# Optimization experiments

Measured on AMD Instinct MI355X. Metric: run time of the kernel, lower is better.

## Reference

```python
import jax, jax.numpy as jnp
import numpy as np

B, S, NN = 16, 512, 8          # batch, spatial nodes, neighbors per node
IN, H, NHEAD = 128, 512, 4     # input_size, hidden_size, n_head


def _forward(inputs, h, c, h_spatial, a_src, w_fg, b_fg, w_ig, b_ig,
             w_ih, w_hh, b_ih, b_hh):
    N = B * S
    x = inputs.reshape(N, IN)
    h = h.reshape(N, H)
    c = c.reshape(N, H)
    hs = h_spatial.reshape(N, NN, H)

    # attention logits: concat(h, neighbor) @ a_src, split to avoid materializing concat
    a_self, a_nb = a_src[:H], a_src[H:]              # [H, NHEAD] each
    attn = h @ a_self                                  # [N, NHEAD]
    attn = attn[:, None, :] + jnp.einsum('nkh,hm->nkm', hs, a_nb)  # [N, NN, NHEAD]
    attn = jnp.where(attn >= 0, attn, 0.2 * attn)      # leaky_relu(0.2)
    attn = jax.nn.softmax(attn, axis=1)                # softmax over neighbors

    # aggregate neighbors per head -> [N, NHEAD*H]
    agg = jnp.einsum('nkm,nkh->nmh', attn, hs).reshape(N, NHEAD * H)

    spatial_f = jax.nn.sigmoid(agg @ w_fg.T + b_fg)    # [N, H]
    spatial_i = jax.nn.sigmoid(agg @ w_ig.T + b_ig)
    h = h * spatial_i
    c = c * spatial_f

    # torch LSTMCell: gate order i, f, g, o
    gates = x @ w_ih.T + b_ih + h @ w_hh.T + b_hh      # [N, 4H]
    i_g, f_g, g_g, o_g = jnp.split(gates, 4, axis=1)
    i_g = jax.nn.sigmoid(i_g)
    f_g = jax.nn.sigmoid(f_g)
    g_g = jnp.tanh(g_g)
    o_g = jax.nn.sigmoid(o_g)
    c_new = f_g * c + i_g * g_g
    h_new = o_g * jnp.tanh(c_new)
    return h_new.reshape(B, S, H), c_new.reshape(B, S, H)


def setup_inputs() -> dict:
    key = jax.random.key(0)
    ks = jax.random.split(key, 16)
    xav = lambda k, shp: jax.random.uniform(
        k, shp, jnp.float32, -1.0, 1.0) * np.sqrt(6.0 / (shp[0] + shp[1]))
    return {
        'inputs': jax.random.normal(ks[0], (B, S, IN), jnp.float32),
        'h': jax.random.normal(ks[1], (B, S, H), jnp.float32),
        'c': jax.random.normal(ks[2], (B, S, H), jnp.float32),
        'h_spatial': jax.random.normal(ks[3], (B, S, NN, H), jnp.float32),
        'a_src': xav(ks[4], (2 * H, NHEAD)),
        'w_fg': jax.random.normal(ks[5], (H, NHEAD * H), jnp.float32) * 0.02,
        'b_fg': jnp.zeros((H,), jnp.float32),
        'w_ig': jax.random.normal(ks[6], (H, NHEAD * H), jnp.float32) * 0.02,
        'b_ig': jnp.zeros((H,), jnp.float32),
        'w_ih': jax.random.normal(ks[7], (4 * H, IN), jnp.float32) * 0.02,
        'w_hh': jax.random.normal(ks[8], (4 * H, H), jnp.float32) * 0.02,
        'b_ih': jnp.zeros((4 * H,), jnp.float32),
        'b_hh': jnp.zeros((4 * H,), jnp.float32),
    }


def reference(inputs, h, c, h_spatial, a_src, w_fg, b_fg, w_ig, b_ig,
              w_ih, w_hh, b_ih, b_hh):
    return _forward(inputs, h, c, h_spatial, a_src, w_fg, b_fg, w_ig, b_ig,
                    w_ih, w_hh, b_ih, b_hh)
```

## Files before the change

kernel.cpp:

```cpp
#include <hip/hip_runtime.h>
#include <hip/hip_bf16.h>
#include <cstdint>
#include <cstddef>

#define N_ROWS 8192
#define HDIM 512
#define INDIM 128
#define NHEADS 4
#define NNB 8

typedef __bf16 bf16_t;
typedef __bf16 bf16x8 __attribute__((ext_vector_type(8)));
typedef __bf16 bf16x4 __attribute__((ext_vector_type(4)));
typedef __bf16 bf16x2 __attribute__((ext_vector_type(2)));
typedef float f32x4 __attribute__((ext_vector_type(4)));

__device__ __forceinline__ float sigmoidf_(float x) { return 1.0f / (1.0f + expf(-x)); }

__device__ __forceinline__ void load_lds16(const void* g, void* l) {
  __builtin_amdgcn_global_load_lds(
      (const __attribute__((address_space(1))) void*)g,
      (__attribute__((address_space(3))) void*)l, 16, 0, 0);
}

__global__ __launch_bounds__(256) void pack_kernel(
    const float* __restrict__ w_fg, const float* __restrict__ w_ig,
    const float* __restrict__ w_ih, const float* __restrict__ w_hh,
    const float* __restrict__ x,
    bf16_t* __restrict__ W1, bf16_t* __restrict__ W2, bf16_t* __restrict__ A2)
{
  int idx = blockIdx.x * 256 + threadIdx.x;
  if (idx < 1024 * 2048) {
    int r = idx >> 11, k = idx & 2047;
    float v = (r < 512) ? w_fg[(size_t)r * 2048 + k] : w_ig[(size_t)(r - 512) * 2048 + k];
    W1[idx] = (bf16_t)v;
    return;
  }
  idx -= 1024 * 2048;
  if (idx < 2048 * 640) {
    int r = idx / 640, k = idx - r * 640;
    float v = (k < 128) ? w_ih[(size_t)r * 128 + k] : w_hh[(size_t)r * 512 + (k - 128)];
    W2[idx] = (bf16_t)v;
    return;
  }
  idx -= 2048 * 640;
  if (idx < N_ROWS * INDIM) {
    int n = idx >> 7, cc = idx & 127;
    A2[(size_t)n * 640 + cc] = (bf16_t)x[idx];
  }
}

__global__ __launch_bounds__(256) void attn_agg_kernel(
    const float* __restrict__ h, const float* __restrict__ hs,
    const float* __restrict__ a_src, bf16_t* __restrict__ agg)
{
  __shared__ float s_hs[NNB][HDIM];
  __shared__ float s_h[HDIM];
  __shared__ float s_logit[NNB][NHEADS];
  __shared__ float s_self[NHEADS];

  const int n = blockIdx.x;
  const int t = threadIdx.x;
  const float* hs_n = hs + (size_t)n * (NNB * HDIM);
  const float* h_n  = h  + (size_t)n * HDIM;

  {
    const float4* s4 = (const float4*)hs_n;
    float4* d4 = (float4*)&s_hs[0][0];
#pragma unroll
    for (int i = 0; i < 4; ++i) d4[t + i * 256] = s4[t + i * 256];
    if (t < HDIM / 4) ((float4*)s_h)[t] = ((const float4*)h_n)[t];
  }
  __syncthreads();

  const int wave = t >> 6, lane = t & 63;
#pragma unroll
  for (int kk = 0; kk < 2; ++kk) {
    const int k = wave * 2 + kk;
    float acc0 = 0.f, acc1 = 0.f, acc2 = 0.f, acc3 = 0.f;
#pragma unroll
    for (int i = 0; i < HDIM / 64; ++i) {
      const int hh = i * 64 + lane;
      const float v = s_hs[k][hh];
      const float4 av = *(const float4*)(a_src + (size_t)(HDIM + hh) * NHEADS);
      acc0 += v * av.x; acc1 += v * av.y; acc2 += v * av.z; acc3 += v * av.w;
    }
    float accs[NHEADS] = {acc0, acc1, acc2, acc3};
#pragma unroll
    for (int m = 0; m < NHEADS; ++m) {
      float a = accs[m];
#pragma unroll
      for (int off = 32; off > 0; off >>= 1) a += __shfl_xor(a, off);
      if (lane == 0) s_logit[k][m] = a;
    }
  }
  if (wave == 0) {
    float acc0 = 0.f, acc1 = 0.f, acc2 = 0.f, acc3 = 0.f;
#pragma unroll
    for (int i = 0; i < HDIM / 64; ++i) {
      const int hh = i * 64 + lane;
      const float v = s_h[hh];
      const float4 av = *(const float4*)(a_src + (size_t)hh * NHEADS);
      acc0 += v * av.x; acc1 += v * av.y; acc2 += v * av.z; acc3 += v * av.w;
    }
    float accs[NHEADS] = {acc0, acc1, acc2, acc3};
#pragma unroll
    for (int m = 0; m < NHEADS; ++m) {
      float a = accs[m];
#pragma unroll
      for (int off = 32; off > 0; off >>= 1) a += __shfl_xor(a, off);
      if (lane == 0) s_self[m] = a;
    }
  }
  __syncthreads();

  float w[NNB][NHEADS];
#pragma unroll
  for (int m = 0; m < NHEADS; ++m) {
    const float sm = s_self[m];
    float mx = -1e30f;
#pragma unroll
    for (int k = 0; k < NNB; ++k) {
      float l = sm + s_logit[k][m];
      l = (l >= 0.f) ? l : 0.2f * l;
      w[k][m] = l;
      mx = fmaxf(mx, l);
    }
    float sum = 0.f;
#pragma unroll
    for (int k = 0; k < NNB; ++k) { const float e = expf(w[k][m] - mx); w[k][m] = e; sum += e; }
    const float inv = 1.f / sum;
#pragma unroll
    for (int k = 0; k < NNB; ++k) w[k][m] *= inv;
  }

  bf16_t* agg_n = agg + (size_t)n * (NHEADS * HDIM);
  const int hh = t * 2;
  float e0[NNB], e1[NNB];
#pragma unroll
  for (int k = 0; k < NNB; ++k) { e0[k] = s_hs[k][hh]; e1[k] = s_hs[k][hh + 1]; }
#pragma unroll
  for (int m = 0; m < NHEADS; ++m) {
    float a0 = 0.f, a1 = 0.f;
#pragma unroll
    for (int k = 0; k < NNB; ++k) { a0 += w[k][m] * e0[k]; a1 += w[k][m] * e1[k]; }
    bf16x2 pk; pk[0] = (bf16_t)a0; pk[1] = (bf16_t)a1;
    *(bf16x2*)(agg_n + m * HDIM + hh) = pk;
  }
}

template <int EPI>
__global__ __launch_bounds__(256) void gemm_kernel(
    const bf16_t* __restrict__ A, int lda,
    const bf16_t* __restrict__ Bt, int ldb, int K,
    const float* __restrict__ p0, const float* __restrict__ p1,
    const float* __restrict__ p2, const float* __restrict__ p3,
    float* __restrict__ q0, bf16_t* __restrict__ q1)
{
  __shared__ bf16_t At[128][32];
  __shared__ bf16_t Bs[128][32];

  const int tid  = threadIdx.x;
  const int wave = tid >> 6, lane = tid & 63;
  const int wr = wave >> 1, wc = wave & 1;
  const int bm0 = blockIdx.x * 128;
  const int bn0 = blockIdx.y * 128;

  f32x4 acc[4][4] = {};

  const int srow = tid >> 2;
  const int scol = (tid & 3) * 8;
  const bf16_t* Ag0 = A  + (size_t)(bm0 + srow)      * lda + scol;
  const bf16_t* Ag1 = A  + (size_t)(bm0 + srow + 64) * lda + scol;
  const bf16_t* Bg0 = Bt + (size_t)(bn0 + srow)      * ldb + scol;
  const bf16_t* Bg1 = Bt + (size_t)(bn0 + srow + 64) * ldb + scol;
  bf16_t* lA0 = &At[srow][scol];
  bf16_t* lA1 = &At[srow + 64][scol];
  bf16_t* lB0 = &Bs[srow][scol];
  bf16_t* lB1 = &Bs[srow + 64][scol];

  const int frow = lane & 15;
  const int kk = (lane >> 4) * 8;

  for (int k0 = 0; k0 < K; k0 += 32) {
    load_lds16(Ag0 + k0, lA0);
    load_lds16(Ag1 + k0, lA1);
    load_lds16(Bg0 + k0, lB0);
    load_lds16(Bg1 + k0, lB1);
    __syncthreads();

    bf16x8 af[4], bf[4];
#pragma unroll
    for (int i = 0; i < 4; ++i) af[i] = *(const bf16x8*)&At[wr * 64 + i * 16 + frow][kk];
#pragma unroll
    for (int j = 0; j < 4; ++j) bf[j] = *(const bf16x8*)&Bs[wc * 64 + j * 16 + frow][kk];
#pragma unroll
    for (int i = 0; i < 4; ++i)
#pragma unroll
      for (int j = 0; j < 4; ++j)
        acc[i][j] = __builtin_amdgcn_mfma_f32_16x16x32_bf16(af[i], bf[j], acc[i][j], 0, 0, 0);
    __syncthreads();
  }

  const int col_in = lane & 15;
  const int row_in = (lane >> 4) * 4;
#pragma unroll
  for (int i = 0; i < 4; ++i) {
#pragma unroll
    for (int j = 0; j < 4; ++j) {
      const int col = bn0 + wc * 64 + j * 16 + col_in;
#pragma unroll
      for (int r = 0; r < 4; ++r) {
        const int row = bm0 + wr * 64 + i * 16 + row_in + r;
        const float v = acc[i][j][r];
        if (EPI == 1) {
          if (col < 512) {
            const float s = sigmoidf_(v + p0[col]);
            q0[(size_t)row * 512 + col] = p2[(size_t)row * 512 + col] * s;
          } else {
            const int jj = col - 512;
            const float s = sigmoidf_(v + p1[jj]);
            q1[(size_t)row * 640 + 128 + jj] = (bf16_t)(p3[(size_t)row * 512 + jj] * s);
          }
        } else {
          q1[(size_t)row * 2048 + col] = (bf16_t)(v + p0[col] + p1[col]);
        }
      }
    }
  }
}

__global__ __launch_bounds__(256) void final_kernel(
    const bf16_t* __restrict__ gates, const float* __restrict__ cprime,
    float* __restrict__ out)
{
  const int idx = blockIdx.x * 256 + threadIdx.x;
  const int n = idx >> 7;
  const int q = (idx & 127) * 4;
  const bf16_t* g = gates + (size_t)n * 2048;
  const bf16x4 gi = *(const bf16x4*)(g + q);
  const bf16x4 gf = *(const bf16x4*)(g + 512 + q);
  const bf16x4 gg = *(const bf16x4*)(g + 1024 + q);
  const bf16x4 go = *(const bf16x4*)(g + 1536 + q);
  const float4 cp = *(const float4*)(cprime + (size_t)n * 512 + q);
  const float cpv[4] = {cp.x, cp.y, cp.z, cp.w};
  float hn[4], cn[4];
#pragma unroll
  for (int r = 0; r < 4; ++r) {
    const float i_g = sigmoidf_((float)gi[r]);
    const float f_g = sigmoidf_((float)gf[r]);
    const float g_g = tanhf((float)gg[r]);
    const float o_g = sigmoidf_((float)go[r]);
    const float c = f_g * cpv[r] + i_g * g_g;
    cn[r] = c;
    hn[r] = o_g * tanhf(c);
  }
  *(float4*)(out + (size_t)n * 512 + q) = *(float4*)hn;
  *(float4*)(out + (size_t)(N_ROWS * HDIM) + (size_t)n * 512 + q) = *(float4*)cn;
}

extern "C" void kernel_launch(void* const* d_in, const int* in_sizes, int n_in,
                              void* d_out, int out_size, void* d_ws, size_t ws_size,
                              hipStream_t stream) {
  const float* x     = (const float*)d_in[0];
  const float* h     = (const float*)d_in[1];
  const float* c     = (const float*)d_in[2];
  const float* hsp   = (const float*)d_in[3];
  const float* a_src = (const float*)d_in[4];
  const float* w_fg  = (const float*)d_in[5];
  const float* b_fg  = (const float*)d_in[6];
  const float* w_ig  = (const float*)d_in[7];
  const float* b_ig  = (const float*)d_in[8];
  const float* w_ih  = (const float*)d_in[9];
  const float* w_hh  = (const float*)d_in[10];
  const float* b_ih  = (const float*)d_in[11];
  const float* b_hh  = (const float*)d_in[12];
  float* out = (float*)d_out;

  uint8_t* ws = (uint8_t*)d_ws;
  bf16_t* agg    = (bf16_t*)(ws);
  bf16_t* W1     = (bf16_t*)(ws + 33554432);
  bf16_t* W2     = (bf16_t*)(ws + 37748736);
  bf16_t* A2     = (bf16_t*)(ws + 40370176);
  float*  cprime = (float*) (ws + 50855936);
  bf16_t* gates  = (bf16_t*)(ws + 67633152);

  pack_kernel<<<17408, 256, 0, stream>>>(w_fg, w_ig, w_ih, w_hh, x, W1, W2, A2);
  attn_agg_kernel<<<N_ROWS, 256, 0, stream>>>(h, hsp, a_src, agg);
  gemm_kernel<1><<<dim3(64, 8), 256, 0, stream>>>(
      agg, 2048, W1, 2048, 2048, b_fg, b_ig, c, h, cprime, A2);
  gemm_kernel<2><<<dim3(64, 16), 256, 0, stream>>>(
      A2, 640, W2, 640, 640, b_ih, b_hh, nullptr, nullptr, nullptr, gates);
  final_kernel<<<4096, 256, 0, stream>>>(gates, cprime, out);
}
```

Measured before the change: 202.8 us.

## Double-buffer GEMM K-loop and fuse LSTM gate epilogue into second GEMM

New measurement: 398.2 us. +96.4%, slower.

```diff
diff --git a/kernel.cpp b/kernel.cpp
--- a/kernel.cpp
+++ b/kernel.cpp
@@ -26,8 +26,10 @@
 __global__ __launch_bounds__(256) void pack_kernel(
     const float* __restrict__ w_fg, const float* __restrict__ w_ig,
     const float* __restrict__ w_ih, const float* __restrict__ w_hh,
+    const float* __restrict__ b_ih, const float* __restrict__ b_hh,
     const float* __restrict__ x,
-    bf16_t* __restrict__ W1, bf16_t* __restrict__ W2, bf16_t* __restrict__ A2)
+    bf16_t* __restrict__ W1, bf16_t* __restrict__ W2i,
+    float* __restrict__ b2, bf16_t* __restrict__ A2)
 {
   int idx = blockIdx.x * 256 + threadIdx.x;
   if (idx < 1024 * 2048) {
@@ -39,11 +41,18 @@
   idx -= 1024 * 2048;
   if (idx < 2048 * 640) {
     int r = idx / 640, k = idx - r * 640;
+    int rp = (r & 511) * 4 + (r >> 9);
     float v = (k < 128) ? w_ih[(size_t)r * 128 + k] : w_hh[(size_t)r * 512 + (k - 128)];
-    W2[idx] = (bf16_t)v;
+    W2i[(size_t)rp * 640 + k] = (bf16_t)v;
     return;
   }
   idx -= 2048 * 640;
+  if (idx < 2048) {
+    int q = idx >> 2, g = idx & 3;
+    b2[idx] = b_ih[g * 512 + q] + b_hh[g * 512 + q];
+    return;
+  }
+  idx -= 2048;
   if (idx < N_ROWS * INDIM) {
     int n = idx >> 7, cc = idx & 127;
     A2[(size_t)n * 640 + cc] = (bf16_t)x[idx];
@@ -150,15 +159,18 @@
 }
 
 template <int EPI>
-__global__ __launch_bounds__(256) void gemm_kernel(
+__global__ __launch_bounds__(256, 2) void gemm2p_kernel(
     const bf16_t* __restrict__ A, int lda,
     const bf16_t* __restrict__ Bt, int ldb, int K,
     const float* __restrict__ p0, const float* __restrict__ p1,
     const float* __restrict__ p2, const float* __restrict__ p3,
-    float* __restrict__ q0, bf16_t* __restrict__ q1)
+    float* __restrict__ q0, bf16_t* __restrict__ q1,
+    float* __restrict__ out)
 {
-  __shared__ bf16_t At[128][32];
-  __shared__ bf16_t Bs[128][32];
+  __shared__ union {
+    struct { bf16_t A[2][128][64]; bf16_t B[2][128][64]; } st;
+    float epi[128][128];
+  } sm;
 
   const int tid  = threadIdx.x;
   const int wave = tid >> 6, lane = tid & 63;
@@ -168,52 +180,71 @@
 
   f32x4 acc[4][4] = {};
 
-  const int srow = tid >> 2;
-  const int scol = (tid & 3) * 8;
-  const bf16_t* Ag0 = A  + (size_t)(bm0 + srow)      * lda + scol;
-  const bf16_t* Ag1 = A  + (size_t)(bm0 + srow + 64) * lda + scol;
-  const bf16_t* Bg0 = Bt + (size_t)(bn0 + srow)      * ldb + scol;
-  const bf16_t* Bg1 = Bt + (size_t)(bn0 + srow + 64) * ldb + scol;
-  bf16_t* lA0 = &At[srow][scol];
-  bf16_t* lA1 = &At[srow + 64][scol];
-  bf16_t* lB0 = &Bs[srow][scol];
-  bf16_t* lB1 = &Bs[srow + 64][scol];
+  const int srow = tid >> 3;
+  const int sch8 = (tid & 7) * 8;
+  const bf16_t* Ag = A  + (size_t)(bm0 + srow) * lda + sch8;
+  const bf16_t* Bg = Bt + (size_t)(bn0 + srow) * ldb + sch8;
 
   const int frow = lane & 15;
-  const int kk = (lane >> 4) * 8;
-
-  for (int k0 = 0; k0 < K; k0 += 32) {
-    load_lds16(Ag0 + k0, lA0);
-    load_lds16(Ag1 + k0, lA1);
-    load_lds16(Bg0 + k0, lB0);
-    load_lds16(Bg1 + k0, lB1);
-    __syncthreads();
-
-    bf16x8 af[4], bf[4];
-#pragma unroll
-    for (int i = 0; i < 4; ++i) af[i] = *(const bf16x8*)&At[wr * 64 + i * 16 + frow][kk];
-#pragma unroll
-    for (int j = 0; j < 4; ++j) bf[j] = *(const bf16x8*)&Bs[wc * 64 + j * 16 + frow][kk];
-#pragma unroll
-    for (int i = 0; i < 4; ++i)
+  const int fk   = (lane >> 4) * 8;
+
+  auto FB = [&]() {
+    __builtin_amdgcn_sched_barrier(0);
+    __builtin_amdgcn_s_barrier();
+    __builtin_amdgcn_sched_barrier(0);
+  };
+  auto STAGE = [&](int buf, int k0) {
+#pragma unroll
+    for (int r = 0; r < 4; ++r)
+      load_lds16(Ag + (size_t)r * 32 * lda + k0, &sm.st.A[buf][srow + 32 * r][sch8]);
+#pragma unroll
+    for (int r = 0; r < 4; ++r)
+      load_lds16(Bg + (size_t)r * 32 * ldb + k0, &sm.st.B[buf][srow + 32 * r][sch8]);
+  };
+  auto COMPUTE = [&](int buf) {
+#pragma unroll
+    for (int kk = 0; kk < 2; ++kk) {
+      bf16x8 af[4], bv[4];
+#pragma unroll
+      for (int i = 0; i < 4; ++i)
+        af[i] = *(const bf16x8*)&sm.st.A[buf][wr * 64 + i * 16 + frow][kk * 32 + fk];
 #pragma unroll
       for (int j = 0; j < 4; ++j)
-        acc[i][j] = __builtin_amdgcn_mfma_f32_16x16x32_bf16(af[i], bf[j], acc[i][j], 0, 0, 0);
-    __syncthreads();
-  }
+        bv[j] = *(const bf16x8*)&sm.st.B[buf][wc * 64 + j * 16 + frow][kk * 32 + fk];
+#pragma unroll
+      for (int i = 0; i < 4; ++i)
+#pragma unroll
+        for (int j = 0; j < 4; ++j)
+          acc[i][j] = __builtin_amdgcn_mfma_f32_16x16x32_bf16(af[i], bv[j], acc[i][j], 0, 0, 0);
+    }
+  };
+
+  const int nt = K >> 6;
+  STAGE(0, 0);
+  for (int t = 0; t < nt - 1; ++t) {
+    STAGE((t + 1) & 1, (t + 1) * 64);
+    asm volatile("s_waitcnt vmcnt(8)" ::: "memory");
+    FB();
+    COMPUTE(t & 1);
+    FB();
+  }
+  asm volatile("s_waitcnt vmcnt(0)" ::: "memory");
+  FB();
+  COMPUTE((nt - 1) & 1);
 
   const int col_in = lane & 15;
   const int row_in = (lane >> 4) * 4;
-#pragma unroll
-  for (int i = 0; i < 4; ++i) {
-#pragma unroll
-    for (int j = 0; j < 4; ++j) {
-      const int col = bn0 + wc * 64 + j * 16 + col_in;
-#pragma unroll
-      for (int r = 0; r < 4; ++r) {
-        const int row = bm0 + wr * 64 + i * 16 + row_in + r;
-        const float v = acc[i][j][r];
-        if (EPI == 1) {
+
+  if (EPI == 1) {
+#pragma unroll
+    for (int i = 0; i < 4; ++i) {
+#pragma unroll
+      for (int j = 0; j < 4; ++j) {
+        const int col = bn0 + wc * 64 + j * 16 + col_in;
+#pragma unroll
+        for (int r = 0; r < 4; ++r) {
+          const int row = bm0 + wr * 64 + i * 16 + row_in + r;
+          const float v = acc[i][j][r];
           if (col < 512) {
             const float s = sigmoidf_(v + p0[col]);
             q0[(size_t)row * 512 + col] = p2[(size_t)row * 512 + col] * s;
@@ -222,41 +253,41 @@
             const float s = sigmoidf_(v + p1[jj]);
             q1[(size_t)row * 640 + 128 + jj] = (bf16_t)(p3[(size_t)row * 512 + jj] * s);
           }
-        } else {
-          q1[(size_t)row * 2048 + col] = (bf16_t)(v + p0[col] + p1[col]);
         }
       }
     }
-  }
-}
-
-__global__ __launch_bounds__(256) void final_kernel(
-    const bf16_t* __restrict__ gates, const float* __restrict__ cprime,
-    float* __restrict__ out)
-{
-  const int idx = blockIdx.x * 256 + threadIdx.x;
-  const int n = idx >> 7;
-  const int q = (idx & 127) * 4;
-  const bf16_t* g = gates + (size_t)n * 2048;
-  const bf16x4 gi = *(const bf16x4*)(g + q);
-  const bf16x4 gf = *(const bf16x4*)(g + 512 + q);
-  const bf16x4 gg = *(const bf16x4*)(g + 1024 + q);
-  const bf16x4 go = *(const bf16x4*)(g + 1536 + q);
-  const float4 cp = *(const float4*)(cprime + (size_t)n * 512 + q);
-  const float cpv[4] = {cp.x, cp.y, cp.z, cp.w};
-  float hn[4], cn[4];
-#pragma unroll
-  for (int r = 0; r < 4; ++r) {
-    const float i_g = sigmoidf_((float)gi[r]);
-    const float f_g = sigmoidf_((float)gf[r]);
-    const float g_g = tanhf((float)gg[r]);
-    const float o_g = sigmoidf_((float)go[r]);
-    const float c = f_g * cpv[r] + i_g * g_g;
-    cn[r] = c;
-    hn[r] = o_g * tanhf(c);
-  }
-  *(float4*)(out + (size_t)n * 512 + q) = *(float4*)hn;
-  *(float4*)(out + (size_t)(N_ROWS * HDIM) + (size_t)n * 512 + q) = *(float4*)cn;
+  } else {
+    FB();
+#pragma unroll
+    for (int i = 0; i < 4; ++i)
+#pragma unroll
+      for (int j = 0; j < 4; ++j)
+#pragma unroll
+        for (int r = 0; r < 4; ++r)
+          sm.epi[wr * 64 + i * 16 + row_in + r][wc * 64 + j * 16 + col_in] = acc[i][j][r];
+    asm volatile("s_waitcnt lgkmcnt(0)" ::: "memory");
+    FB();
+    const int q0i = bn0 >> 2;
+#pragma unroll
+    for (int pass = 0; pass < 16; ++pass) {
+      const int idx = pass * 256 + tid;
+      const int r  = idx >> 5;
+      const int qi = idx & 31;
+      const float4 g4 = *(const float4*)&sm.epi[r][qi * 4];
+      const float4 bb = *(const float4*)&p0[(size_t)(q0i + qi) * 4];
+      const int grow = bm0 + r;
+      const int q    = q0i + qi;
+      const float cp = p1[(size_t)grow * 512 + q];
+      const float ig = sigmoidf_(g4.x + bb.x);
+      const float fg = sigmoidf_(g4.y + bb.y);
+      const float gg = tanhf(g4.z + bb.z);
+      const float og = sigmoidf_(g4.w + bb.w);
+      const float cn = fg * cp + ig * gg;
+      const float hn = og * tanhf(cn);
+      out[(size_t)grow * 512 + q] = hn;
+      out[(size_t)N_ROWS * 512 + (size_t)grow * 512 + q] = cn;
+    }
+  }
 }
 
 extern "C" void kernel_launch(void* const* d_in, const int* in_sizes, int n_in,
@@ -280,16 +311,16 @@
   uint8_t* ws = (uint8_t*)d_ws;
   bf16_t* agg    = (bf16_t*)(ws);
   bf16_t* W1     = (bf16_t*)(ws + 33554432);
-  bf16_t* W2     = (bf16_t*)(ws + 37748736);
-  bf16_t* A2     = (bf16_t*)(ws + 40370176);
-  float*  cprime = (float*) (ws + 50855936);
-  bf16_t* gates  = (bf16_t*)(ws + 67633152);
-
-  pack_kernel<<<17408, 256, 0, stream>>>(w_fg, w_ig, w_ih, w_hh, x, W1, W2, A2);
+  bf16_t* W2i    = (bf16_t*)(ws + 37748736);
+  float*  b2     = (float*) (ws + 40370176);
+  bf16_t* A2     = (bf16_t*)(ws + 40378368);
+  float*  cprime = (float*) (ws + 50864128);
+
+  pack_kernel<<<17416, 256, 0, stream>>>(w_fg, w_ig, w_ih, w_hh, b_ih, b_hh, x,
+                                         W1, W2i, b2, A2);
   attn_agg_kernel<<<N_ROWS, 256, 0, stream>>>(h, hsp, a_src, agg);
-  gemm_kernel<1><<<dim3(64, 8), 256, 0, stream>>>(
-      agg, 2048, W1, 2048, 2048, b_fg, b_ig, c, h, cprime, A2);
-  gemm_kernel<2><<<dim3(64, 16), 256, 0, stream>>>(
-      A2, 640, W2, 640, 640, b_ih, b_hh, nullptr, nullptr, nullptr, gates);
-  final_kernel<<<4096, 256, 0, stream>>>(gates, cprime, out);
-}
+  gemm2p_kernel<1><<<dim3(64, 8), 256, 0, stream>>>(
+      agg, 2048, W1, 2048, 2048, b_fg, b_ig, c, h, cprime, A2, nullptr);
+  gemm2p_kernel<2><<<dim3(64, 16), 256, 0, stream>>>(
+      A2, 640, W2i, 640, 640, b2, cprime, nullptr, nullptr, nullptr, nullptr, out);
+}
```
